# Performance work log

Hardware: AMD Instinct MI355X
Metric: run time of the kernel (lower is better)

Reference implementation:

```python
import jax, jax.numpy as jnp
import numpy as np

N = 20000      # nodes
E = 640000     # edges (before self loops)
IN = 256       # in_channels == out_channels (forced by classifier size 4*in)
H1, C1 = 8, 16   # conv1: heads=8, out=16 -> concat 128
H2, C2 = 1, 256  # conv2: heads=1, out=out_channels
B = 4096       # article pairs
NEG_SLOPE = 0.2  # PyG GATv2Conv default negative_slope


def setup_inputs() -> dict:
    key = jax.random.key(0)
    ks = jax.random.split(key, 24)
    s = 0.05
    inp = {
        "gnn_x": jax.random.normal(ks[0], (N, IN), jnp.float32),
        "vanilla_x": jax.random.normal(ks[1], (N, IN), jnp.float32),
        "edge_src": jax.random.randint(ks[2], (E,), 0, N, jnp.int32),
        "edge_dst": jax.random.randint(ks[3], (E,), 0, N, jnp.int32),
        "a1_idx": jax.random.randint(ks[4], (B,), 0, N, jnp.int64),
        "a2_idx": jax.random.randint(ks[5], (B,), 0, N, jnp.int64),
        # conv1 params (lin_l, lin_r, att, bias)
        "Wl1": jax.random.normal(ks[6], (IN, H1 * C1), jnp.float32) * s,
        "bl1": jnp.zeros((H1 * C1,), jnp.float32),
        "Wr1": jax.random.normal(ks[7], (IN, H1 * C1), jnp.float32) * s,
        "br1": jnp.zeros((H1 * C1,), jnp.float32),
        "att1": jax.random.normal(ks[8], (H1, C1), jnp.float32) * s,
        "bias1": jnp.zeros((H1 * C1,), jnp.float32),
        # conv2 params
        "Wl2": jax.random.normal(ks[9], (H1 * C1, H2 * C2), jnp.float32) * s,
        "bl2": jnp.zeros((H2 * C2,), jnp.float32),
        "Wr2": jax.random.normal(ks[10], (H1 * C1, H2 * C2), jnp.float32) * s,
        "br2": jnp.zeros((H2 * C2,), jnp.float32),
        "att2": jax.random.normal(ks[11], (H2, C2), jnp.float32) * s,
        "bias2": jnp.zeros((H2 * C2,), jnp.float32),
        # classifier
        "Wc": jax.random.normal(ks[12], (4 * IN, 1), jnp.float32) * s,
        "bc": jnp.zeros((1,), jnp.float32),
    }
    return inp


def _gatv2_layer(x, src, dst, Wl, bl, Wr, br, att, bias):
    """GATv2Conv: x_l = lin_l(x)[src], x_r = lin_r(x)[dst];
    e = att . leaky_relu(x_l + x_r); segment softmax over dst; scatter-add x_l*alpha."""
    n = x.shape[0]
    h, c = att.shape
    xl = (x @ Wl + bl).reshape(n, h, c)
    xr = (x @ Wr + br).reshape(n, h, c)
    # per-edge attention logits [E, H]
    e = jnp.einsum('ehc,hc->eh', jax.nn.leaky_relu(xl[src] + xr[dst], NEG_SLOPE), att)
    # segment softmax over destination nodes (self loops guarantee non-empty segments)
    emax = jax.ops.segment_max(e, dst, num_segments=n)
    ex = jnp.exp(e - emax[dst])
    denom = jax.ops.segment_sum(ex, dst, num_segments=n)
    alpha = ex / denom[dst]                      # [E, H]
    out = jax.ops.segment_sum(alpha[:, :, None] * xl[src], dst, num_segments=n)  # [N,H,C]
    return out.reshape(n, h * c) + bias          # concat=True (heads=1 identical)


def reference(gnn_x, vanilla_x, Wl1, bl1, Wr1, br1, att1, bias1,
              Wl2, bl2, Wr2, br2, att2, bias2, Wc, bc,
              edge_src, edge_dst, a1_idx, a2_idx):
    n = gnn_x.shape[0]
    loops = jnp.arange(n, dtype=edge_src.dtype)
    src = jnp.concatenate([edge_src, loops])     # PyG add_self_loops=True
    dst = jnp.concatenate([edge_dst, loops])
    x = _gatv2_layer(gnn_x, src, dst, Wl1, bl1, Wr1, br1, att1, bias1)
    x = jax.nn.relu(x)
    x = _gatv2_layer(x, src, dst, Wl2, bl2, Wr2, br2, att2, bias2)
    combined = jnp.concatenate(
        [vanilla_x[a1_idx], vanilla_x[a2_idx], x[a1_idx], x[a2_idx]], axis=1)  # [B, 4*IN]
    logits = combined @ Wc + bc                  # [B, 1]
    return logits
```

## Files before the change

kernel.cpp:

```cpp
#include <hip/hip_runtime.h>
#include <math.h>

#define N_NODES 20000
#define M_PAD   20032
#define E_EDGES 640000
#define ET (E_EDGES + N_NODES)
#define IN_CH 256
#define D1 128
#define D2 256
#define BPAIRS 4096
#define NEG 0.2f
#define LOG2E 1.4426950408889634f

#define XCONV_BLOCKS 5008
#define WCONV_BLOCKS 512
#define HIST_BLOCKS  ((ET + 255) / 256)

#if __has_builtin(__builtin_amdgcn_exp2f)
#define EXP2F(x) __builtin_amdgcn_exp2f(x)
#else
#define EXP2F(x) exp2f(x)
#endif

typedef __bf16 bf16x8 __attribute__((ext_vector_type(8)));
typedef float  f32x4  __attribute__((ext_vector_type(4)));
typedef float  f32x2  __attribute__((ext_vector_type(2)));

__device__ __forceinline__ unsigned short f2b(float f) {
    unsigned int u = __float_as_uint(f);
    unsigned int r = u + 0x7FFFu + ((u >> 16) & 1u);
    return (unsigned short)(r >> 16);
}
__device__ __forceinline__ f32x2 up2(unsigned int u) {
    f32x2 r;
    r.x = __uint_as_float(u << 16);
    r.y = __uint_as_float(u & 0xFFFF0000u);
    return r;
}
__device__ __forceinline__ f32x2 lrelu2(f32x2 s) {
    return __builtin_elementwise_max(s, s * NEG);
}


__global__ void prep_kernel(
        const float* __restrict__ gnn_x,
        const float* __restrict__ Wl1, const float* __restrict__ Wr1,
        const float* __restrict__ Wl2, const float* __restrict__ Wr2,
        const int* __restrict__ edge_dst,
        unsigned short* __restrict__ xb,
        unsigned short* __restrict__ wt1l, unsigned short* __restrict__ wt1r,
        unsigned short* __restrict__ wt2l, unsigned short* __restrict__ wt2r,
        int* __restrict__ count, int* __restrict__ rank) {
    int bid = blockIdx.x;
    if (bid < XCONV_BLOCKS) {
        int e0 = (bid * 256 + threadIdx.x) * 4;
        int row = e0 >> 8;
        ushort4 o;
        if (row < N_NODES) {
            float4 v = *(const float4*)(gnn_x + e0);
            o.x = f2b(v.x); o.y = f2b(v.y); o.z = f2b(v.z); o.w = f2b(v.w);
        } else {
            o.x = o.y = o.z = o.w = 0;
        }
        *(ushort4*)(xb + e0) = o;
    } else if (bid < XCONV_BLOCKS + WCONV_BLOCKS) {
        int idx = (bid - XCONV_BLOCKS) * 256 + threadIdx.x;
        int seg = idx >> 15;
        int r = idx & 32767;
        const float* W;
        unsigned short* Wt;
        int k, n, K;
        if (seg < 2) {
            W = seg ? Wr1 : Wl1; Wt = seg ? wt1r : wt1l;
            k = r >> 7; n = r & 127; K = IN_CH;
        } else {
            W = (seg & 1) ? Wr2 : Wl2; Wt = (seg & 1) ? wt2r : wt2l;
            k = r >> 8; n = r & 255; K = D1;
        }
        Wt[n * K + k] = f2b(W[r]);
    } else {
        int e = (bid - XCONV_BLOCKS - WCONV_BLOCKS) * 256 + threadIdx.x;
        if (e >= ET) return;
        int dst = (e < E_EDGES) ? edge_dst[e] : (e - E_EDGES);
        rank[e] = atomicAdd(&count[dst], 1);
    }
}


__global__ __launch_bounds__(1024) void scan_kernel(const int* __restrict__ count,
                                                    int* __restrict__ offsets) {
    const int PER = 20;
    int t = threadIdx.x;
    int base = t * PER;
    int local[PER];
    int sum = 0;
#pragma unroll
    for (int i = 0; i < PER; i++) {
        int idx = base + i;
        int v = (idx < N_NODES) ? count[idx] : 0;
        local[i] = sum;
        sum += v;
    }
    int lane = t & 63, wave = t >> 6;
    int s = sum;
#pragma unroll
    for (int off = 1; off < 64; off <<= 1) {
        int x = __shfl_up(s, off);
        if (lane >= off) s += x;
    }
    __shared__ int wsum[16];
    __shared__ int wpre[16];
    if (lane == 63) wsum[wave] = s;
    __syncthreads();
    if (t == 0) {
        int acc = 0;
        for (int w = 0; w < 16; w++) { wpre[w] = acc; acc += wsum[w]; }
        offsets[N_NODES] = acc;
    }
    __syncthreads();
    int thread_excl = wpre[wave] + (s - sum);
#pragma unroll
    for (int i = 0; i < PER; i++) {
        int idx = base + i;
        if (idx < N_NODES) offsets[idx] = thread_excl + local[i];
    }
}

__global__ void scatter_kernel(const int* __restrict__ edge_src,
                               const int* __restrict__ edge_dst,
                               const int* __restrict__ rank,
                               const int* __restrict__ offsets,
                               int* __restrict__ sorted_src) {
    int e = blockIdx.x * blockDim.x + threadIdx.x;
    if (e >= ET) return;
    int dst = (e < E_EDGES) ? edge_dst[e] : (e - E_EDGES);
    int src = (e < E_EDGES) ? edge_src[e] : (e - E_EDGES);
    sorted_src[offsets[dst] + rank[e]] = src;
}


template <int K>
__global__ __launch_bounds__(256) void dual_gemm_mfma_kernel(
        const unsigned short* __restrict__ A,
        const unsigned short* __restrict__ Wtl,
        const unsigned short* __restrict__ Wtr,
        const float* __restrict__ bl, const float* __restrict__ br,
        unsigned short* __restrict__ Yl, unsigned short* __restrict__ Yr,
        int M, int NOUT) {
    int wave = threadIdx.x >> 6;
    int lane = threadIdx.x & 63;
    int row0 = blockIdx.x * 64;
    int col0 = (blockIdx.y * 4 + wave) * 16;
    int rsub = lane & 15;
    int koff = (lane >> 4) * 8;

    const unsigned short* ap  = A   + (size_t)(row0 + rsub) * K + koff;
    const unsigned short* bpl = Wtl + (size_t)(col0 + rsub) * K + koff;
    const unsigned short* bpr = Wtr + (size_t)(col0 + rsub) * K + koff;

    f32x4 l0 = {0.f, 0.f, 0.f, 0.f};
    f32x4 l1 = l0, l2 = l0, l3 = l0, r0 = l0, r1 = l0, r2 = l0, r3 = l0;

#pragma unroll
    for (int kb = 0; kb < K; kb += 32) {
        bf16x8 bfl = *(const bf16x8*)(bpl + kb);
        bf16x8 bfr = *(const bf16x8*)(bpr + kb);
        bf16x8 a0 = *(const bf16x8*)(ap + kb);
        bf16x8 a1 = *(const bf16x8*)(ap + 16 * K + kb);
        bf16x8 a2 = *(const bf16x8*)(ap + 32 * K + kb);
        bf16x8 a3 = *(const bf16x8*)(ap + 48 * K + kb);
        l0 = __builtin_amdgcn_mfma_f32_16x16x32_bf16(a0, bfl, l0, 0, 0, 0);
        r0 = __builtin_amdgcn_mfma_f32_16x16x32_bf16(a0, bfr, r0, 0, 0, 0);
        l1 = __builtin_amdgcn_mfma_f32_16x16x32_bf16(a1, bfl, l1, 0, 0, 0);
        r1 = __builtin_amdgcn_mfma_f32_16x16x32_bf16(a1, bfr, r1, 0, 0, 0);
        l2 = __builtin_amdgcn_mfma_f32_16x16x32_bf16(a2, bfl, l2, 0, 0, 0);
        r2 = __builtin_amdgcn_mfma_f32_16x16x32_bf16(a2, bfr, r2, 0, 0, 0);
        l3 = __builtin_amdgcn_mfma_f32_16x16x32_bf16(a3, bfl, l3, 0, 0, 0);
        r3 = __builtin_amdgcn_mfma_f32_16x16x32_bf16(a3, bfr, r3, 0, 0, 0);
    }

    int colg = col0 + rsub;
    float bvl = bl[colg];
    float bvr = br[colg];
    int rbase = row0 + (lane >> 4) * 4;
#pragma unroll
    for (int t = 0; t < 4; t++) {
        f32x4 al = (t == 0) ? l0 : (t == 1) ? l1 : (t == 2) ? l2 : l3;
        f32x4 ar = (t == 0) ? r0 : (t == 1) ? r1 : (t == 2) ? r2 : r3;
#pragma unroll
        for (int r = 0; r < 4; r++) {
            int row = rbase + t * 16 + r;
            if (row < M) {
                Yl[(size_t)row * NOUT + colg] = f2b(al[r] + bvl);
                Yr[(size_t)row * NOUT + colg] = f2b(ar[r] + bvr);
            }
        }
    }
}


__global__ __launch_bounds__(256) void aggregate1_kernel(
        const unsigned short* __restrict__ xl1, const unsigned short* __restrict__ xr1,
        const float* __restrict__ att1, const float* __restrict__ bias1,
        const int* __restrict__ offsets, const int* __restrict__ sorted_src,
        unsigned short* __restrict__ x1) {
    int wave = threadIdx.x >> 6;
    int lane = threadIdx.x & 63;
    int q = lane >> 4;
    int ql = lane & 15;
    int dst = blockIdx.x * 4 + wave;
    if (dst >= M_PAD) return;
    int c0 = ql * 8;
    if (dst >= N_NODES) {
        if (q == 0) {
            uint4 z; z.x = z.y = z.z = z.w = 0;
            *(uint4*)(x1 + (size_t)dst * D1 + c0) = z;
        }
        return;
    }

    uint4 xu = *(const uint4*)(xr1 + (size_t)dst * D1 + c0);
    f32x2 xr[4] = {up2(xu.x), up2(xu.y), up2(xu.z), up2(xu.w)};
    float4 aa0 = *(const float4*)(att1 + c0);
    float4 aa1 = *(const float4*)(att1 + c0 + 4);
    f32x2 att[4];
    att[0].x = aa0.x * LOG2E; att[0].y = aa0.y * LOG2E;
    att[1].x = aa0.z * LOG2E; att[1].y = aa0.w * LOG2E;
    att[2].x = aa1.x * LOG2E; att[2].y = aa1.y * LOG2E;
    att[3].x = aa1.z * LOG2E; att[3].y = aa1.w * LOG2E;

    int beg = offsets[dst], end = offsets[dst + 1];
    const unsigned short* base = xl1 + c0;

    float l = 0.f;
    f32x2 acc[4] = {{0.f,0.f},{0.f,0.f},{0.f,0.f},{0.f,0.f}};

    int i = beg;
    int s0 = sorted_src[min(i + q, end - 1)];
    uint4 g0 = *(const uint4*)(base + (size_t)s0 * D1);
    while (true) {
        int inext = i + 4;
        bool more = inext < end;
        uint4 g1;
        if (more) {
            int s1 = sorted_src[min(inext + q, end - 1)];
            g1 = *(const uint4*)(base + (size_t)s1 * D1);
        }
        bool act = (i + q) < end;
        f32x2 v0 = up2(g0.x), v1 = up2(g0.y), v2 = up2(g0.z), v3 = up2(g0.w);
        f32x2 p2 = att[0] * lrelu2(v0 + xr[0]);
        p2 += att[1] * lrelu2(v1 + xr[1]);
        p2 += att[2] * lrelu2(v2 + xr[2]);
        p2 += att[3] * lrelu2(v3 + xr[3]);
        float p = p2.x + p2.y;
        p += __shfl_xor(p, 1);
        float w = act ? EXP2F(p) : 0.f;
        l += w;
        acc[0] += w * v0; acc[1] += w * v1; acc[2] += w * v2; acc[3] += w * v3;
        if (!more) break;
        i = inext; g0 = g1;
    }
    l += __shfl_xor(l, 16);
    l += __shfl_xor(l, 32);
#pragma unroll
    for (int j = 0; j < 4; j++) {
        f32x2 t;
        t.x = __shfl_xor(acc[j].x, 16); t.y = __shfl_xor(acc[j].y, 16);
        acc[j] += t;
        t.x = __shfl_xor(acc[j].x, 32); t.y = __shfl_xor(acc[j].y, 32);
        acc[j] += t;
    }
    if (q == 0) {
        float inv = 1.f / l;
        float4 bb0 = *(const float4*)(bias1 + c0);
        float4 bb1 = *(const float4*)(bias1 + c0 + 4);
        unsigned short o[8];
        o[0] = f2b(fmaxf(acc[0].x * inv + bb0.x, 0.f));
        o[1] = f2b(fmaxf(acc[0].y * inv + bb0.y, 0.f));
        o[2] = f2b(fmaxf(acc[1].x * inv + bb0.z, 0.f));
        o[3] = f2b(fmaxf(acc[1].y * inv + bb0.w, 0.f));
        o[4] = f2b(fmaxf(acc[2].x * inv + bb1.x, 0.f));
        o[5] = f2b(fmaxf(acc[2].y * inv + bb1.y, 0.f));
        o[6] = f2b(fmaxf(acc[3].x * inv + bb1.z, 0.f));
        o[7] = f2b(fmaxf(acc[3].y * inv + bb1.w, 0.f));
        uint4 ov;
        ov.x = (unsigned int)o[0] | ((unsigned int)o[1] << 16);
        ov.y = (unsigned int)o[2] | ((unsigned int)o[3] << 16);
        ov.z = (unsigned int)o[4] | ((unsigned int)o[5] << 16);
        ov.w = (unsigned int)o[6] | ((unsigned int)o[7] << 16);
        *(uint4*)(x1 + (size_t)dst * D1 + c0) = ov;
    }
}


__global__ __launch_bounds__(256) void aggregate2_kernel(
        const unsigned short* __restrict__ xl2, const unsigned short* __restrict__ xr2,
        const float* __restrict__ att2, const float* __restrict__ bias2,
        const int* __restrict__ offsets, const int* __restrict__ sorted_src,
        float* __restrict__ x2) {
    int wave = threadIdx.x >> 6;
    int lane = threadIdx.x & 63;
    int half = lane >> 5;
    int hl = lane & 31;
    int dst = blockIdx.x * 4 + wave;
    if (dst >= N_NODES) return;
    int c0 = hl * 8;

    uint4 xu = *(const uint4*)(xr2 + (size_t)dst * D2 + c0);
    f32x2 xr[4] = {up2(xu.x), up2(xu.y), up2(xu.z), up2(xu.w)};
    float4 aa0 = *(const float4*)(att2 + c0);
    float4 aa1 = *(const float4*)(att2 + c0 + 4);
    f32x2 att[4];
    att[0].x = aa0.x * LOG2E; att[0].y = aa0.y * LOG2E;
    att[1].x = aa0.z * LOG2E; att[1].y = aa0.w * LOG2E;
    att[2].x = aa1.x * LOG2E; att[2].y = aa1.y * LOG2E;
    att[3].x = aa1.z * LOG2E; att[3].y = aa1.w * LOG2E;

    int beg = offsets[dst], end = offsets[dst + 1];
    const unsigned short* base = xl2 + c0;

    float l = 0.f;
    f32x2 acc[4] = {{0.f,0.f},{0.f,0.f},{0.f,0.f},{0.f,0.f}};

    int i = beg;
    int sA = sorted_src[min(i + half, end - 1)];
    int sB = sorted_src[min(i + 2 + half, end - 1)];
    uint4 gA = *(const uint4*)(base + (size_t)sA * D2);
    uint4 gB = *(const uint4*)(base + (size_t)sB * D2);
    while (true) {
        int inext = i + 4;
        bool more = inext < end;
        uint4 gA2, gB2;
        if (more) {
            int sA2 = sorted_src[min(inext + half, end - 1)];
            int sB2 = sorted_src[min(inext + 2 + half, end - 1)];
            gA2 = *(const uint4*)(base + (size_t)sA2 * D2);
            gB2 = *(const uint4*)(base + (size_t)sB2 * D2);
        }
        bool actA = (i + half) < end;
        bool actB = (i + 2 + half) < end;

        f32x2 vA0 = up2(gA.x), vA1 = up2(gA.y), vA2 = up2(gA.z), vA3 = up2(gA.w);
        f32x2 vB0 = up2(gB.x), vB1 = up2(gB.y), vB2 = up2(gB.z), vB3 = up2(gB.w);
        f32x2 pA2 = att[0] * lrelu2(vA0 + xr[0]);
        f32x2 pB2 = att[0] * lrelu2(vB0 + xr[0]);
        pA2 += att[1] * lrelu2(vA1 + xr[1]);
        pB2 += att[1] * lrelu2(vB1 + xr[1]);
        pA2 += att[2] * lrelu2(vA2 + xr[2]);
        pB2 += att[2] * lrelu2(vB2 + xr[2]);
        pA2 += att[3] * lrelu2(vA3 + xr[3]);
        pB2 += att[3] * lrelu2(vB3 + xr[3]);
        float pA = pA2.x + pA2.y;
        float pB = pB2.x + pB2.y;
        pA += __shfl_xor(pA, 1);  pB += __shfl_xor(pB, 1);
        pA += __shfl_xor(pA, 2);  pB += __shfl_xor(pB, 2);
        pA += __shfl_xor(pA, 4);  pB += __shfl_xor(pB, 4);
        pA += __shfl_xor(pA, 8);  pB += __shfl_xor(pB, 8);
        pA += __shfl_xor(pA, 16); pB += __shfl_xor(pB, 16);
        float wA = actA ? EXP2F(pA) : 0.f;
        float wB = actB ? EXP2F(pB) : 0.f;
        l += wA + wB;
        acc[0] += wA * vA0 + wB * vB0;
        acc[1] += wA * vA1 + wB * vB1;
        acc[2] += wA * vA2 + wB * vB2;
        acc[3] += wA * vA3 + wB * vB3;
        if (!more) break;
        i = inext; gA = gA2; gB = gB2;
    }
    l += __shfl_xor(l, 32);
#pragma unroll
    for (int j = 0; j < 4; j++) {
        f32x2 t;
        t.x = __shfl_xor(acc[j].x, 32); t.y = __shfl_xor(acc[j].y, 32);
        acc[j] += t;
    }
    if (half == 0) {
        float inv = 1.f / l;
        float4 bb0 = *(const float4*)(bias2 + c0);
        float4 bb1 = *(const float4*)(bias2 + c0 + 4);
        float4 o0, o1;
        o0.x = acc[0].x * inv + bb0.x;
        o0.y = acc[0].y * inv + bb0.y;
        o0.z = acc[1].x * inv + bb0.z;
        o0.w = acc[1].y * inv + bb0.w;
        o1.x = acc[2].x * inv + bb1.x;
        o1.y = acc[2].y * inv + bb1.y;
        o1.z = acc[3].x * inv + bb1.z;
        o1.w = acc[3].y * inv + bb1.w;
        *(float4*)(x2 + (size_t)dst * D2 + c0) = o0;
        *(float4*)(x2 + (size_t)dst * D2 + c0 + 4) = o1;
    }
}


__global__ __launch_bounds__(256) void classifier_kernel(
        const float* __restrict__ vanilla_x, const float* __restrict__ x2,
        const int* __restrict__ a1_raw, const int* __restrict__ a2_raw,
        const float* __restrict__ Wc, const float* __restrict__ bc,
        float* __restrict__ out) {
    int b = blockIdx.x;
    int t = threadIdx.x;

    __shared__ int stride_s;
    if (t == 0) {
        bool i64 = true;
        for (int i = 1; i < 63; i += 2) i64 = i64 && (a1_raw[i] == 0);
        stride_s = i64 ? 2 : 1;
    }
    __syncthreads();
    int stride = stride_s;
    int a1 = a1_raw[(long)b * stride];
    int a2 = a2_raw[(long)b * stride];

    float s = vanilla_x[a1 * IN_CH + t] * Wc[t]
            + vanilla_x[a2 * IN_CH + t] * Wc[IN_CH + t]
            + x2[a1 * D2 + t] * Wc[2 * IN_CH + t]
            + x2[a2 * D2 + t] * Wc[3 * IN_CH + t];
    s += __shfl_xor(s, 1);
    s += __shfl_xor(s, 2);
    s += __shfl_xor(s, 4);
    s += __shfl_xor(s, 8);
    s += __shfl_xor(s, 16);
    s += __shfl_xor(s, 32);
    __shared__ float part[4];
    if ((t & 63) == 0) part[t >> 6] = s;
    __syncthreads();
    if (t == 0) out[b] = part[0] + part[1] + part[2] + part[3] + bc[0];
}


extern "C" void kernel_launch(void* const* d_in, const int* in_sizes, int n_in,
                              void* d_out, int out_size, void* d_ws, size_t ws_size,
                              hipStream_t stream) {
    const float* gnn_x     = (const float*)d_in[0];
    const float* vanilla_x = (const float*)d_in[1];
    const int*   edge_src  = (const int*)d_in[2];
    const int*   edge_dst  = (const int*)d_in[3];
    const int*   a1_idx    = (const int*)d_in[4];
    const int*   a2_idx    = (const int*)d_in[5];
    const float* Wl1   = (const float*)d_in[6];
    const float* bl1   = (const float*)d_in[7];
    const float* Wr1   = (const float*)d_in[8];
    const float* br1   = (const float*)d_in[9];
    const float* att1  = (const float*)d_in[10];
    const float* bias1 = (const float*)d_in[11];
    const float* Wl2   = (const float*)d_in[12];
    const float* bl2   = (const float*)d_in[13];
    const float* Wr2   = (const float*)d_in[14];
    const float* br2   = (const float*)d_in[15];
    const float* att2  = (const float*)d_in[16];
    const float* bias2 = (const float*)d_in[17];
    const float* Wc    = (const float*)d_in[18];
    const float* bc    = (const float*)d_in[19];
    float* out = (float*)d_out;

    char* p = (char*)d_ws;
    unsigned short* xb   = (unsigned short*)p; p += (size_t)M_PAD * IN_CH * 2;
    unsigned short* x1b  = (unsigned short*)p; p += (size_t)M_PAD * D1 * 2;
    unsigned short* xl1b = (unsigned short*)p; p += (size_t)N_NODES * D1 * 2;
    unsigned short* xr1b = (unsigned short*)p; p += (size_t)N_NODES * D1 * 2;
    unsigned short* xl2b = (unsigned short*)p; p += (size_t)N_NODES * D2 * 2;
    unsigned short* xr2b = (unsigned short*)p; p += (size_t)N_NODES * D2 * 2;
    unsigned short* wt1l = (unsigned short*)p; p += (size_t)D1 * IN_CH * 2;
    unsigned short* wt1r = (unsigned short*)p; p += (size_t)D1 * IN_CH * 2;
    unsigned short* wt2l = (unsigned short*)p; p += (size_t)D2 * D1 * 2;
    unsigned short* wt2r = (unsigned short*)p; p += (size_t)D2 * D1 * 2;
    float* x2 = (float*)p; p += (size_t)N_NODES * D2 * 4;
    int* count      = (int*)p; p += (size_t)N_NODES * 4;
    int* offsets    = (int*)p; p += (size_t)(N_NODES + 4) * 4;
    int* rank       = (int*)p; p += (size_t)ET * 4;
    int* sorted_src = (int*)p; p += (size_t)ET * 4;

    hipMemsetAsync(count, 0, (size_t)N_NODES * sizeof(int), stream);

    prep_kernel<<<XCONV_BLOCKS + WCONV_BLOCKS + HIST_BLOCKS, 256, 0, stream>>>(
        gnn_x, Wl1, Wr1, Wl2, Wr2, edge_dst,
        xb, wt1l, wt1r, wt2l, wt2r, count, rank);
    scan_kernel<<<1, 1024, 0, stream>>>(count, offsets);
    scatter_kernel<<<HIST_BLOCKS, 256, 0, stream>>>(
        edge_src, edge_dst, rank, offsets, sorted_src);

    dim3 g1(M_PAD / 64, D1 / 64);
    dual_gemm_mfma_kernel<IN_CH><<<g1, 256, 0, stream>>>(
        xb, wt1l, wt1r, bl1, br1, xl1b, xr1b, N_NODES, D1);
    aggregate1_kernel<<<M_PAD / 4, 256, 0, stream>>>(
        xl1b, xr1b, att1, bias1, offsets, sorted_src, x1b);

    dim3 g2(M_PAD / 64, D2 / 64);
    dual_gemm_mfma_kernel<D1><<<g2, 256, 0, stream>>>(
        x1b, wt2l, wt2r, bl2, br2, xl2b, xr2b, N_NODES, D2);
    aggregate2_kernel<<<(N_NODES + 3) / 4, 256, 0, stream>>>(
        xl2b, xr2b, att2, bias2, offsets, sorted_src, x2);

    classifier_kernel<<<BPAIRS, 256, 0, stream>>>(
        vanilla_x, x2, a1_idx, a2_idx, Wc, bc, out);
}
```

Measured before the change: 298.4 us.

## Skip layer-2 aggregation for nodes not referenced by classifier pairs

Marks the nodes referenced by a1_idx/a2_idx in the prep kernel and has aggregate2 return early for unmarked destination nodes, since only those rows of x2 are read by the classifier. At most 8192 of the 20000 nodes need layer-2 aggregation. The aggregate2 inner loop is also rewritten with scalar arrays and separate remainder loops instead of clamped software-prefetched loads, which drops the next-iteration prefetch. The memset is extended to zero the new mark array.

Result: faster. 280.7 us (-5.9%).

```diff
diff --git a/kernel.cpp b/kernel.cpp
--- a/kernel.cpp
+++ b/kernel.cpp
@@ -15,6 +15,7 @@
 #define XCONV_BLOCKS 5008
 #define WCONV_BLOCKS 512
 #define HIST_BLOCKS  ((ET + 255) / 256)
+#define MARK_BLOCKS  (2 * BPAIRS / 256)
 
 #if __has_builtin(__builtin_amdgcn_exp2f)
 #define EXP2F(x) __builtin_amdgcn_exp2f(x)
@@ -40,6 +41,14 @@
 __device__ __forceinline__ f32x2 lrelu2(f32x2 s) {
     return __builtin_elementwise_max(s, s * NEG);
 }
+__device__ __forceinline__ float lrelu(float s) { return fmaxf(s, NEG * s); }
+
+__device__ __forceinline__ void unpack8(uint4 u, float* v) {
+    v[0] = __uint_as_float(u.x << 16); v[1] = __uint_as_float(u.x & 0xFFFF0000u);
+    v[2] = __uint_as_float(u.y << 16); v[3] = __uint_as_float(u.y & 0xFFFF0000u);
+    v[4] = __uint_as_float(u.z << 16); v[5] = __uint_as_float(u.z & 0xFFFF0000u);
+    v[6] = __uint_as_float(u.w << 16); v[7] = __uint_as_float(u.w & 0xFFFF0000u);
+}
 
 
 __global__ void prep_kernel(
@@ -47,10 +56,12 @@
         const float* __restrict__ Wl1, const float* __restrict__ Wr1,
         const float* __restrict__ Wl2, const float* __restrict__ Wr2,
         const int* __restrict__ edge_dst,
+        const int* __restrict__ a1_raw, const int* __restrict__ a2_raw,
         unsigned short* __restrict__ xb,
         unsigned short* __restrict__ wt1l, unsigned short* __restrict__ wt1r,
         unsigned short* __restrict__ wt2l, unsigned short* __restrict__ wt2r,
-        int* __restrict__ count, int* __restrict__ rank) {
+        int* __restrict__ count, int* __restrict__ rank,
+        int* __restrict__ mark) {
     int bid = blockIdx.x;
     if (bid < XCONV_BLOCKS) {
         int e0 = (bid * 256 + threadIdx.x) * 4;
@@ -78,11 +89,24 @@
             k = r >> 8; n = r & 255; K = D1;
         }
         Wt[n * K + k] = f2b(W[r]);
-    } else {
+    } else if (bid < XCONV_BLOCKS + WCONV_BLOCKS + HIST_BLOCKS) {
         int e = (bid - XCONV_BLOCKS - WCONV_BLOCKS) * 256 + threadIdx.x;
         if (e >= ET) return;
         int dst = (e < E_EDGES) ? edge_dst[e] : (e - E_EDGES);
         rank[e] = atomicAdd(&count[dst], 1);
+    } else {
+        int idx = (bid - XCONV_BLOCKS - WCONV_BLOCKS - HIST_BLOCKS) * 256
+                + threadIdx.x;
+        __shared__ int stride_s;
+        if (threadIdx.x == 0) {
+            bool i64 = true;
+            for (int i = 1; i < 63; i += 2) i64 = i64 && (a1_raw[i] == 0);
+            stride_s = i64 ? 2 : 1;
+        }
+        __syncthreads();
+        int stride = stride_s;
+        if (idx < BPAIRS) mark[a1_raw[(long)idx * stride]] = 1;
+        else mark[a2_raw[(long)(idx - BPAIRS) * stride]] = 1;
     }
 }
 
@@ -297,6 +321,7 @@
         const unsigned short* __restrict__ xl2, const unsigned short* __restrict__ xr2,
         const float* __restrict__ att2, const float* __restrict__ bias2,
         const int* __restrict__ offsets, const int* __restrict__ sorted_src,
+        const int* __restrict__ mark,
         float* __restrict__ x2) {
     int wave = threadIdx.x >> 6;
     int lane = threadIdx.x & 63;
@@ -304,89 +329,90 @@
     int hl = lane & 31;
     int dst = blockIdx.x * 4 + wave;
     if (dst >= N_NODES) return;
+    if (!mark[dst]) return;
     int c0 = hl * 8;
 
-    uint4 xu = *(const uint4*)(xr2 + (size_t)dst * D2 + c0);
-    f32x2 xr[4] = {up2(xu.x), up2(xu.y), up2(xu.z), up2(xu.w)};
-    float4 aa0 = *(const float4*)(att2 + c0);
-    float4 aa1 = *(const float4*)(att2 + c0 + 4);
-    f32x2 att[4];
-    att[0].x = aa0.x * LOG2E; att[0].y = aa0.y * LOG2E;
-    att[1].x = aa0.z * LOG2E; att[1].y = aa0.w * LOG2E;
-    att[2].x = aa1.x * LOG2E; att[2].y = aa1.y * LOG2E;
-    att[3].x = aa1.z * LOG2E; att[3].y = aa1.w * LOG2E;
-
+    float xr[8], att[8];
+    unpack8(*(const uint4*)(xr2 + (size_t)dst * D2 + c0), xr);
+#pragma unroll
+    for (int j = 0; j < 8; j++) att[j] = att2[c0 + j] * LOG2E;
     int beg = offsets[dst], end = offsets[dst + 1];
-    const unsigned short* base = xl2 + c0;
 
     float l = 0.f;
-    f32x2 acc[4] = {{0.f,0.f},{0.f,0.f},{0.f,0.f},{0.f,0.f}};
+    float acc[8];
+#pragma unroll
+    for (int j = 0; j < 8; j++) acc[j] = 0.f;
 
     int i = beg;
-    int sA = sorted_src[min(i + half, end - 1)];
-    int sB = sorted_src[min(i + 2 + half, end - 1)];
-    uint4 gA = *(const uint4*)(base + (size_t)sA * D2);
-    uint4 gB = *(const uint4*)(base + (size_t)sB * D2);
-    while (true) {
-        int inext = i + 4;
-        bool more = inext < end;
-        uint4 gA2, gB2;
-        if (more) {
-            int sA2 = sorted_src[min(inext + half, end - 1)];
-            int sB2 = sorted_src[min(inext + 2 + half, end - 1)];
-            gA2 = *(const uint4*)(base + (size_t)sA2 * D2);
-            gB2 = *(const uint4*)(base + (size_t)sB2 * D2);
-        }
-        bool actA = (i + half) < end;
-        bool actB = (i + 2 + half) < end;
-
-        f32x2 vA0 = up2(gA.x), vA1 = up2(gA.y), vA2 = up2(gA.z), vA3 = up2(gA.w);
-        f32x2 vB0 = up2(gB.x), vB1 = up2(gB.y), vB2 = up2(gB.z), vB3 = up2(gB.w);
-        f32x2 pA2 = att[0] * lrelu2(vA0 + xr[0]);
-        f32x2 pB2 = att[0] * lrelu2(vB0 + xr[0]);
-        pA2 += att[1] * lrelu2(vA1 + xr[1]);
-        pB2 += att[1] * lrelu2(vB1 + xr[1]);
-        pA2 += att[2] * lrelu2(vA2 + xr[2]);
-        pB2 += att[2] * lrelu2(vB2 + xr[2]);
-        pA2 += att[3] * lrelu2(vA3 + xr[3]);
-        pB2 += att[3] * lrelu2(vB3 + xr[3]);
-        float pA = pA2.x + pA2.y;
-        float pB = pB2.x + pB2.y;
+    for (; i + 4 <= end; i += 4) {
+        int sA = sorted_src[i + half];
+        int sB = sorted_src[i + 2 + half];
+        float vA[8], vB[8];
+        unpack8(*(const uint4*)(xl2 + (size_t)sA * D2 + c0), vA);
+        unpack8(*(const uint4*)(xl2 + (size_t)sB * D2 + c0), vB);
+        float pA = 0.f, pB = 0.f;
+#pragma unroll
+        for (int j = 0; j < 8; j++) pA = fmaf(att[j], lrelu(vA[j] + xr[j]), pA);
+#pragma unroll
+        for (int j = 0; j < 8; j++) pB = fmaf(att[j], lrelu(vB[j] + xr[j]), pB);
         pA += __shfl_xor(pA, 1);  pB += __shfl_xor(pB, 1);
         pA += __shfl_xor(pA, 2);  pB += __shfl_xor(pB, 2);
         pA += __shfl_xor(pA, 4);  pB += __shfl_xor(pB, 4);
         pA += __shfl_xor(pA, 8);  pB += __shfl_xor(pB, 8);
         pA += __shfl_xor(pA, 16); pB += __shfl_xor(pB, 16);
-        float wA = actA ? EXP2F(pA) : 0.f;
-        float wB = actB ? EXP2F(pB) : 0.f;
+        float wA = EXP2F(pA), wB = EXP2F(pB);
         l += wA + wB;
-        acc[0] += wA * vA0 + wB * vB0;
-        acc[1] += wA * vA1 + wB * vB1;
-        acc[2] += wA * vA2 + wB * vB2;
-        acc[3] += wA * vA3 + wB * vB3;
-        if (!more) break;
-        i = inext; gA = gA2; gB = gB2;
+#pragma unroll
+        for (int j = 0; j < 8; j++) acc[j] += wA * vA[j] + wB * vB[j];
+    }
+    for (; i + 2 <= end; i += 2) {
+        int sA = sorted_src[i + half];
+        float vA[8];
+        unpack8(*(const uint4*)(xl2 + (size_t)sA * D2 + c0), vA);
+        float pA = 0.f;
+#pragma unroll
+        for (int j = 0; j < 8; j++) pA = fmaf(att[j], lrelu(vA[j] + xr[j]), pA);
+        pA += __shfl_xor(pA, 1);
+        pA += __shfl_xor(pA, 2);
+        pA += __shfl_xor(pA, 4);
+        pA += __shfl_xor(pA, 8);
+        pA += __shfl_xor(pA, 16);
+        float wA = EXP2F(pA);
+        l += wA;
+#pragma unroll
+        for (int j = 0; j < 8; j++) acc[j] += wA * vA[j];
+    }
+    if (i < end && half == 0) {
+        int sA = sorted_src[i];
+        float vA[8];
+        unpack8(*(const uint4*)(xl2 + (size_t)sA * D2 + c0), vA);
+        float pA = 0.f;
+#pragma unroll
+        for (int j = 0; j < 8; j++) pA = fmaf(att[j], lrelu(vA[j] + xr[j]), pA);
+        pA += __shfl_xor(pA, 1);
+        pA += __shfl_xor(pA, 2);
+        pA += __shfl_xor(pA, 4);
+        pA += __shfl_xor(pA, 8);
+        pA += __shfl_xor(pA, 16);
+        float wA = EXP2F(pA);
+        l += wA;
+#pragma unroll
+        for (int j = 0; j < 8; j++) acc[j] += wA * vA[j];
     }
     l += __shfl_xor(l, 32);
 #pragma unroll
-    for (int j = 0; j < 4; j++) {
-        f32x2 t;
-        t.x = __shfl_xor(acc[j].x, 32); t.y = __shfl_xor(acc[j].y, 32);
-        acc[j] += t;
-    }
+    for (int j = 0; j < 8; j++) acc[j] += __shfl_xor(acc[j], 32);
     if (half == 0) {
         float inv = 1.f / l;
-        float4 bb0 = *(const float4*)(bias2 + c0);
-        float4 bb1 = *(const float4*)(bias2 + c0 + 4);
         float4 o0, o1;
-        o0.x = acc[0].x * inv + bb0.x;
-        o0.y = acc[0].y * inv + bb0.y;
-        o0.z = acc[1].x * inv + bb0.z;
-        o0.w = acc[1].y * inv + bb0.w;
-        o1.x = acc[2].x * inv + bb1.x;
-        o1.y = acc[2].y * inv + bb1.y;
-        o1.z = acc[3].x * inv + bb1.z;
-        o1.w = acc[3].y * inv + bb1.w;
+        o0.x = acc[0] * inv + bias2[c0 + 0];
+        o0.y = acc[1] * inv + bias2[c0 + 1];
+        o0.z = acc[2] * inv + bias2[c0 + 2];
+        o0.w = acc[3] * inv + bias2[c0 + 3];
+        o1.x = acc[4] * inv + bias2[c0 + 4];
+        o1.y = acc[5] * inv + bias2[c0 + 5];
+        o1.z = acc[6] * inv + bias2[c0 + 6];
+        o1.w = acc[7] * inv + bias2[c0 + 7];
         *(float4*)(x2 + (size_t)dst * D2 + c0) = o0;
         *(float4*)(x2 + (size_t)dst * D2 + c0 + 4) = o1;
     }
@@ -467,15 +493,17 @@
     unsigned short* wt2r = (unsigned short*)p; p += (size_t)D2 * D1 * 2;
     float* x2 = (float*)p; p += (size_t)N_NODES * D2 * 4;
     int* count      = (int*)p; p += (size_t)N_NODES * 4;
+    int* mark       = (int*)p; p += (size_t)N_NODES * 4;
     int* offsets    = (int*)p; p += (size_t)(N_NODES + 4) * 4;
     int* rank       = (int*)p; p += (size_t)ET * 4;
     int* sorted_src = (int*)p; p += (size_t)ET * 4;
 
-    hipMemsetAsync(count, 0, (size_t)N_NODES * sizeof(int), stream);
-
-    prep_kernel<<<XCONV_BLOCKS + WCONV_BLOCKS + HIST_BLOCKS, 256, 0, stream>>>(
-        gnn_x, Wl1, Wr1, Wl2, Wr2, edge_dst,
-        xb, wt1l, wt1r, wt2l, wt2r, count, rank);
+    hipMemsetAsync(count, 0, (size_t)2 * N_NODES * sizeof(int), stream);
+
+    prep_kernel<<<XCONV_BLOCKS + WCONV_BLOCKS + HIST_BLOCKS + MARK_BLOCKS,
+                  256, 0, stream>>>(
+        gnn_x, Wl1, Wr1, Wl2, Wr2, edge_dst, a1_idx, a2_idx,
+        xb, wt1l, wt1r, wt2l, wt2r, count, rank, mark);
     scan_kernel<<<1, 1024, 0, stream>>>(count, offsets);
     scatter_kernel<<<HIST_BLOCKS, 256, 0, stream>>>(
         edge_src, edge_dst, rank, offsets, sorted_src);
@@ -490,7 +518,7 @@
     dual_gemm_mfma_kernel<D1><<<g2, 256, 0, stream>>>(
         x1b, wt2l, wt2r, bl2, br2, xl2b, xr2b, N_NODES, D2);
     aggregate2_kernel<<<(N_NODES + 3) / 4, 256, 0, stream>>>(
-        xl2b, xr2b, att2, bias2, offsets, sorted_src, x2);
+        xl2b, xr2b, att2, bias2, offsets, sorted_src, mark, x2);
 
     classifier_kernel<<<BPAIRS, 256, 0, stream>>>(
         vanilla_x, x2, a1_idx, a2_idx, Wc, bc, out);
```
